# Optimization experiments

Hardware: AMD Instinct MI355X
Metric: run time of the kernel (lower is better)

## Reference

```python
import jax, jax.numpy as jnp
import numpy as np

E4M3_MAX = 448.0
CHUNKS = 4  # module init: chunks=4, seg_mode='weight', equal chunksizes of out//chunks


def fp8_quant(v):
    # Simulate real e4m3 quantization: saturate then round-to-nearest e4m3, back to f32.
    return jnp.clip(v, -E4M3_MAX, E4M3_MAX).astype(jnp.float8_e4m3fn).astype(jnp.float32)


def setup_inputs() -> dict:
    key = jax.random.key(0)
    k1, k2, k3 = jax.random.split(key, 3)
    B, S, IN, OUT = 4, 4096, 4096, 4096
    x = jax.random.normal(k1, (B, S, IN), jnp.float32)
    w = jax.random.normal(k2, (OUT, IN), jnp.float32) * 0.02
    bias = jax.random.normal(k3, (OUT,), jnp.float32) * 0.01
    # Max-calibrated per-tensor scales (quantizer.scale from calibration)
    in_scale = jnp.max(jnp.abs(x)) / E4M3_MAX          # scalar
    wc = w.reshape(CHUNKS, OUT // CHUNKS, IN)
    w_scales = jnp.max(jnp.abs(wc), axis=(1, 2)) / E4M3_MAX  # [CHUNKS]
    return {"x": x, "w": w, "bias": bias, "in_scale": in_scale, "w_scales": w_scales}


def reference(x, w, bias, in_scale, w_scales):
    # seg_mode='weight': split weight along out_features into CHUNKS equal chunks,
    # run scaled e4m3 GEMM per chunk, concat outputs along out dim, add bias.
    OUT, IN = w.shape
    wc = w.reshape(CHUNKS, OUT // CHUNKS, IN)                 # [c, oc, i]
    xq = fp8_quant(x / in_scale)                              # [b, s, i]
    wq = fp8_quant(wc / w_scales[:, None, None])              # [c, oc, i]
    # out_i = (xq @ wq_i^T) * in_scale * w_scale_i  (dequant fused into GEMM epilogue)
    out = jnp.einsum('bsi,coi->bsco', xq, wq)
    out = out * (in_scale * w_scales)[None, None, :, None]
    out = out.reshape(x.shape[0], x.shape[1], OUT)            # concat chunk outputs
    return out + bias
```

## Files before the change

kernel.cpp:

```cpp
#include <hip/hip_runtime.h>
#include <stdint.h>

#define E4M3_MAX 448.0f

typedef float f32x4 __attribute__((ext_vector_type(4)));
typedef int   i32x4 __attribute__((ext_vector_type(4)));
typedef int   i32x8 __attribute__((ext_vector_type(8)));

__device__ __forceinline__ void gload_lds16(const void* g, void* l) {
    __builtin_amdgcn_global_load_lds(
        (__attribute__((address_space(1))) void*)(void*)g,
        (__attribute__((address_space(3))) void*)l,
        16, 0, 0);
}

__device__ __forceinline__ uint32_t quant4(float a, float b, float c, float d) {
    a = fminf(fmaxf(a, -E4M3_MAX), E4M3_MAX);
    b = fminf(fmaxf(b, -E4M3_MAX), E4M3_MAX);
    c = fminf(fmaxf(c, -E4M3_MAX), E4M3_MAX);
    d = fminf(fmaxf(d, -E4M3_MAX), E4M3_MAX);
    int q = 0;
    q = __builtin_amdgcn_cvt_pk_fp8_f32(a, b, q, false);
    q = __builtin_amdgcn_cvt_pk_fp8_f32(c, d, q, true);
    return (uint32_t)q;
}

__global__ void quant_x_kernel(const float* __restrict__ x,
                               const float* __restrict__ scale_p,
                               uint4* __restrict__ xq, int n16) {
    const float inv = 1.0f / scale_p[0];
    const int stride = gridDim.x * blockDim.x;
    for (int i = blockIdx.x * blockDim.x + threadIdx.x; i < n16; i += stride) {
        const float4* p = (const float4*)x + (size_t)i * 4;
        float4 v0 = p[0], v1 = p[1], v2 = p[2], v3 = p[3];
        uint4 q;
        q.x = quant4(v0.x * inv, v0.y * inv, v0.z * inv, v0.w * inv);
        q.y = quant4(v1.x * inv, v1.y * inv, v1.z * inv, v1.w * inv);
        q.z = quant4(v2.x * inv, v2.y * inv, v2.z * inv, v2.w * inv);
        q.w = quant4(v3.x * inv, v3.y * inv, v3.z * inv, v3.w * inv);
        xq[i] = q;
    }
}

__global__ void quant_w_kernel(const float* __restrict__ w,
                               const float* __restrict__ wsc,
                               uint8_t* __restrict__ wq,
                               int Nrows, int K, int chunkRows) {
    const int nkt = K >> 7;
    const int n32 = Nrows * (K >> 5);
    const int stride = gridDim.x * blockDim.x;
    for (int i = blockIdx.x * blockDim.x + threadIdx.x; i < n32; i += stride) {
        const int n  = i % Nrows;
        const int k0 = (i / Nrows) << 5;
        const float inv = 1.0f / wsc[n / chunkRows];
        const float4* p = (const float4*)(w + (size_t)n * K + k0);
        uint4 qa, qb;
        {
            float4 v0 = p[0], v1 = p[1], v2 = p[2], v3 = p[3];
            qa.x = quant4(v0.x * inv, v0.y * inv, v0.z * inv, v0.w * inv);
            qa.y = quant4(v1.x * inv, v1.y * inv, v1.z * inv, v1.w * inv);
            qa.z = quant4(v2.x * inv, v2.y * inv, v2.z * inv, v2.w * inv);
            qa.w = quant4(v3.x * inv, v3.y * inv, v3.z * inv, v3.w * inv);
        }
        {
            float4 v0 = p[4], v1 = p[5], v2 = p[6], v3 = p[7];
            qb.x = quant4(v0.x * inv, v0.y * inv, v0.z * inv, v0.w * inv);
            qb.y = quant4(v1.x * inv, v1.y * inv, v1.z * inv, v1.w * inv);
            qb.z = quant4(v2.x * inv, v2.y * inv, v2.z * inv, v2.w * inv);
            qb.w = quant4(v3.x * inv, v3.y * inv, v3.z * inv, v3.w * inv);
        }
        const int kt = k0 >> 7, kg = (k0 >> 5) & 3, r = n & 15, nf = n >> 4;
        uint8_t* dst = wq + (((size_t)nf * nkt + kt) * 64 + kg * 16 + r) * 32;
        *(uint4*)dst = qa;
        *(uint4*)(dst + 16) = qb;
    }
}

__device__ __forceinline__ i32x8 read_frag(const uint8_t* base, int o0, int o1) {
    i32x4 lo = *(const i32x4*)(base + o0);
    i32x4 hi = *(const i32x4*)(base + o1);
    return __builtin_shufflevector(lo, hi, 0, 1, 2, 3, 4, 5, 6, 7);
}

#define MFMA_MX(a, b, c) \
    __builtin_amdgcn_mfma_scale_f32_16x16x128_f8f6f4( \
        (a), (b), (c), 0, 0, 0, 0x7F7F7F7F, 0, 0x7F7F7F7F)

#define WAIT_LGKM(n)                                            \
    do {                                                        \
        asm volatile("s_waitcnt lgkmcnt(" #n ")" ::: "memory"); \
        __builtin_amdgcn_sched_barrier(0);                      \
    } while (0)

#define BM 256
#define BN 256
#define BKB 128

__global__ __launch_bounds__(512, 2) void gemm_fp8_kernel(
    const uint8_t* __restrict__ Aq, const uint8_t* __restrict__ Bq,
    const float* __restrict__ bias, const float* __restrict__ isp,
    const float* __restrict__ wsc, float* __restrict__ out,
    int M, int N, int K, int ocPerChunk) {
    __shared__ __align__(16) uint8_t As[2][BM * BKB];

    const int tid  = threadIdx.x;
    const int lane = tid & 63;
    const int wid  = tid >> 6;
    const int wm   = wid >> 2;
    const int wn   = wid & 3;

    const int nbx   = N / BN;
    const int nby   = M / BM;
    const int chunk = nby >> 3;
    const int xcd   = blockIdx.x & 7;
    const int local = blockIdx.x >> 3;
    const int bx    = local / chunk;
    const int by    = xcd * chunk + (local % chunk);
    const int m0    = by * BM;
    const int n0    = bx * BN;

    const int lr   = lane & 15;
    const int sw   = (lr & 7) << 4;
    const int off0 = ((lane >> 4) * 32) ^ sw;
    const int off1 = off0 ^ 16;

    f32x4 acc[8][4] = {};

    const int nkt = K / BKB;

    const uint8_t* bbase =
        Bq + ((size_t)((n0 >> 4) + wn * 4) * nkt) * 2048 + lane * 32;

    auto stage = [&](int b, int kt) {
#pragma unroll
        for (int i = 0; i < 4; ++i) {
            const int idx = i * 512 + tid;
            const int row = idx >> 3;
            const int col = ((idx & 7) * 16) ^ ((row & 7) << 4);
            gload_lds16(Aq + (size_t)(m0 + row) * K + kt + col,
                        &As[b][0] + idx * 16);
        }
    };

    stage(0, 0);
    asm volatile("s_waitcnt vmcnt(0)" ::: "memory");
    __builtin_amdgcn_s_barrier();

    for (int t = 0; t < nkt; ++t) {
        const int cur = t & 1;
        const uint8_t* pa = &As[cur][0] + (wm * 128 + lr) * BKB;

        i32x8 bv[4];
#pragma unroll
        for (int ni = 0; ni < 4; ni++) {
            const uint8_t* p = bbase + ((size_t)ni * nkt + t) * 2048;
            i32x4 lo = *(const i32x4*)p;
            i32x4 hi = *(const i32x4*)(p + 16);
            bv[ni] = __builtin_shufflevector(lo, hi, 0, 1, 2, 3, 4, 5, 6, 7);
        }
        __builtin_amdgcn_sched_barrier(0);

        i32x8 a0 = read_frag(pa,            off0, off1);
        i32x8 a1 = read_frag(pa + 16 * BKB, off0, off1);
        i32x8 a2 = read_frag(pa + 32 * BKB, off0, off1);
        i32x8 a3 = read_frag(pa + 48 * BKB, off0, off1);
        __builtin_amdgcn_sched_barrier(0);
        const bool pre = (t + 1 < nkt);
        if (pre) stage(cur ^ 1, (t + 1) * BKB);
        __builtin_amdgcn_sched_barrier(0);

        if (pre) asm volatile("s_waitcnt vmcnt(4)" ::: "memory");
        else     asm volatile("s_waitcnt vmcnt(0)" ::: "memory");
        WAIT_LGKM(4);
        __builtin_amdgcn_s_setprio(1);
#pragma unroll
        for (int ni = 0; ni < 4; ni++) {
            acc[0][ni] = MFMA_MX(a0, bv[ni], acc[0][ni]);
            acc[1][ni] = MFMA_MX(a1, bv[ni], acc[1][ni]);
        }
        __builtin_amdgcn_s_setprio(0);

        i32x8 a4 = read_frag(pa + 64 * BKB, off0, off1);
        i32x8 a5 = read_frag(pa + 80 * BKB, off0, off1);
        WAIT_LGKM(4);
        __builtin_amdgcn_s_setprio(1);
#pragma unroll
        for (int ni = 0; ni < 4; ni++) {
            acc[2][ni] = MFMA_MX(a2, bv[ni], acc[2][ni]);
            acc[3][ni] = MFMA_MX(a3, bv[ni], acc[3][ni]);
        }
        __builtin_amdgcn_s_setprio(0);

        i32x8 a6 = read_frag(pa + 96 * BKB,  off0, off1);
        i32x8 a7 = read_frag(pa + 112 * BKB, off0, off1);
        WAIT_LGKM(4);
        __builtin_amdgcn_s_setprio(1);
#pragma unroll
        for (int ni = 0; ni < 4; ni++) {
            acc[4][ni] = MFMA_MX(a4, bv[ni], acc[4][ni]);
            acc[5][ni] = MFMA_MX(a5, bv[ni], acc[5][ni]);
        }
        __builtin_amdgcn_s_setprio(0);

        WAIT_LGKM(0);
        __builtin_amdgcn_s_setprio(1);
#pragma unroll
        for (int ni = 0; ni < 4; ni++) {
            acc[6][ni] = MFMA_MX(a6, bv[ni], acc[6][ni]);
            acc[7][ni] = MFMA_MX(a7, bv[ni], acc[7][ni]);
        }
        __builtin_amdgcn_s_setprio(0);

        asm volatile("s_waitcnt vmcnt(0)" ::: "memory");
        __builtin_amdgcn_sched_barrier(0);
        __builtin_amdgcn_s_barrier();
    }

    const float is = isp[0];
#pragma unroll
    for (int ni = 0; ni < 4; ni++) {
        const int cidx = n0 + wn * 64 + ni * 16 + lr;
        const float sc = is * wsc[cidx / ocPerChunk];
        const float bs = bias[cidx];
#pragma unroll
        for (int mi = 0; mi < 8; mi++) {
            const int rbase = m0 + wm * 128 + mi * 16 + (lane >> 4) * 4;
#pragma unroll
            for (int j = 0; j < 4; j++)
                out[(size_t)(rbase + j) * N + cidx] = acc[mi][ni][j] * sc + bs;
        }
    }
}

extern "C" void kernel_launch(void* const* d_in, const int* in_sizes, int n_in,
                              void* d_out, int out_size, void* d_ws, size_t ws_size,
                              hipStream_t stream) {
    const float* x        = (const float*)d_in[0];
    const float* w        = (const float*)d_in[1];
    const float* bias     = (const float*)d_in[2];
    const float* in_scale = (const float*)d_in[3];
    const float* w_scales = (const float*)d_in[4];
    float* out = (float*)d_out;

    const int N = in_sizes[2];
    const int K = in_sizes[1] / N;
    const int M = in_sizes[0] / K;
    const int CHUNKS = in_sizes[4];
    const int ocPerChunk = N / CHUNKS;

    uint8_t* xq = (uint8_t*)d_ws;
    uint8_t* wq = xq + (size_t)M * K;

    const int xn16 = (int)(((size_t)M * K) / 16);

    quant_x_kernel<<<2048, 256, 0, stream>>>(x, in_scale, (uint4*)xq, xn16);
    quant_w_kernel<<<2048, 256, 0, stream>>>(w, w_scales, wq, N, K, ocPerChunk);

    const int nblk = (M / BM) * (N / BN);
    gemm_fp8_kernel<<<dim3(nblk), 512, 0, stream>>>(xq, wq, bias, in_scale,
                                                    w_scales, out, M, N, K,
                                                    ocPerChunk);
}
```

Before: 422.2 us.

## Prefetch B fragments one K-tile ahead into double-buffered registers

B-operand fragments are now loaded from global memory one K-tile ahead, into a second set of registers, alongside the A-tile LDS stage. The loop is unrolled by two so the current and next register sets swap roles each half. The vmcnt waits are retuned so MFMAs no longer wait on the current tile's B loads, which hides global latency that used to be exposed every iteration. The cost is 32 more live VGPRs per lane under a launch bound of 2 blocks of 512 threads, which risks spills or lower occupancy. The loop also now assumes the number of K tiles is even.

```diff
diff --git a/kernel.cpp b/kernel.cpp
--- a/kernel.cpp
+++ b/kernel.cpp
@@ -82,6 +82,12 @@
     return __builtin_shufflevector(lo, hi, 0, 1, 2, 3, 4, 5, 6, 7);
 }
 
+__device__ __forceinline__ i32x8 load_bfrag(const uint8_t* p) {
+    i32x4 lo = *(const i32x4*)p;
+    i32x4 hi = *(const i32x4*)(p + 16);
+    return __builtin_shufflevector(lo, hi, 0, 1, 2, 3, 4, 5, 6, 7);
+}
+
 #define MFMA_MX(a, b, c) \
     __builtin_amdgcn_mfma_scale_f32_16x16x128_f8f6f4( \
         (a), (b), (c), 0, 0, 0, 0x7F7F7F7F, 0, 0x7F7F7F7F)
@@ -92,9 +98,88 @@
         __builtin_amdgcn_sched_barrier(0);                      \
     } while (0)
 
+#define WAIT_VM(n)                                              \
+    do {                                                        \
+        asm volatile("s_waitcnt vmcnt(" #n ")" ::: "memory");   \
+        __builtin_amdgcn_sched_barrier(0);                      \
+    } while (0)
+
 #define BM 256
 #define BN 256
 #define BKB 128
+
+#define TILE_ITER(T, BC0, BC1, BC2, BC3, BN0, BN1, BN2, BN3)                   \
+    do {                                                                       \
+        const int  cur = (T) & 1;                                              \
+        const bool pre = ((T) + 1 < nkt);                                      \
+        const uint8_t* pa = &As[cur][0] + (wm * 128 + lr) * BKB;               \
+        if (pre) {                                                             \
+            stage(cur ^ 1, ((T) + 1) * BKB);                                   \
+            __builtin_amdgcn_sched_barrier(0);                                 \
+            const uint8_t* bb = bbase + (size_t)((T) + 1) * 2048;              \
+            BN0 = load_bfrag(bb);                                              \
+            BN1 = load_bfrag(bb + (size_t)nkt * 2048);                         \
+            BN2 = load_bfrag(bb + (size_t)nkt * 4096);                         \
+            BN3 = load_bfrag(bb + (size_t)nkt * 6144);                         \
+            __builtin_amdgcn_sched_barrier(0);                                 \
+        }                                                                      \
+                            \
+        i32x8 a0 = read_frag(pa,            off0, off1);                       \
+        i32x8 a1 = read_frag(pa + 16 * BKB, off0, off1);                       \
+        i32x8 a2 = read_frag(pa + 32 * BKB, off0, off1);                       \
+        i32x8 a3 = read_frag(pa + 48 * BKB, off0, off1);                       \
+        if (pre) { WAIT_VM(12); } else { WAIT_VM(0); }                         \
+        WAIT_LGKM(4);                        \
+        __builtin_amdgcn_s_setprio(1);                                         \
+        acc[0][0] = MFMA_MX(a0, BC0, acc[0][0]);                               \
+        acc[0][1] = MFMA_MX(a0, BC1, acc[0][1]);                               \
+        acc[0][2] = MFMA_MX(a0, BC2, acc[0][2]);                               \
+        acc[0][3] = MFMA_MX(a0, BC3, acc[0][3]);                               \
+        acc[1][0] = MFMA_MX(a1, BC0, acc[1][0]);                               \
+        acc[1][1] = MFMA_MX(a1, BC1, acc[1][1]);                               \
+        acc[1][2] = MFMA_MX(a1, BC2, acc[1][2]);                               \
+        acc[1][3] = MFMA_MX(a1, BC3, acc[1][3]);                               \
+        __builtin_amdgcn_s_setprio(0);                                         \
+        i32x8 a4 = read_frag(pa + 64 * BKB, off0, off1);                       \
+        i32x8 a5 = read_frag(pa + 80 * BKB, off0, off1);                       \
+        WAIT_LGKM(4);                        \
+        __builtin_amdgcn_s_setprio(1);                                         \
+        acc[2][0] = MFMA_MX(a2, BC0, acc[2][0]);                               \
+        acc[2][1] = MFMA_MX(a2, BC1, acc[2][1]);                               \
+        acc[2][2] = MFMA_MX(a2, BC2, acc[2][2]);                               \
+        acc[2][3] = MFMA_MX(a2, BC3, acc[2][3]);                               \
+        acc[3][0] = MFMA_MX(a3, BC0, acc[3][0]);                               \
+        acc[3][1] = MFMA_MX(a3, BC1, acc[3][1]);                               \
+        acc[3][2] = MFMA_MX(a3, BC2, acc[3][2]);                               \
+        acc[3][3] = MFMA_MX(a3, BC3, acc[3][3]);                               \
+        __builtin_amdgcn_s_setprio(0);                                         \
+        i32x8 a6 = read_frag(pa + 96 * BKB,  off0, off1);                      \
+        i32x8 a7 = read_frag(pa + 112 * BKB, off0, off1);                      \
+        WAIT_LGKM(4);                        \
+        __builtin_amdgcn_s_setprio(1);                                         \
+        acc[4][0] = MFMA_MX(a4, BC0, acc[4][0]);                               \
+        acc[4][1] = MFMA_MX(a4, BC1, acc[4][1]);                               \
+        acc[4][2] = MFMA_MX(a4, BC2, acc[4][2]);                               \
+        acc[4][3] = MFMA_MX(a4, BC3, acc[4][3]);                               \
+        acc[5][0] = MFMA_MX(a5, BC0, acc[5][0]);                               \
+        acc[5][1] = MFMA_MX(a5, BC1, acc[5][1]);                               \
+        acc[5][2] = MFMA_MX(a5, BC2, acc[5][2]);                               \
+        acc[5][3] = MFMA_MX(a5, BC3, acc[5][3]);                               \
+        __builtin_amdgcn_s_setprio(0);                                         \
+        WAIT_LGKM(0);                                         \
+        __builtin_amdgcn_s_setprio(1);                                         \
+        acc[6][0] = MFMA_MX(a6, BC0, acc[6][0]);                               \
+        acc[6][1] = MFMA_MX(a6, BC1, acc[6][1]);                               \
+        acc[6][2] = MFMA_MX(a6, BC2, acc[6][2]);                               \
+        acc[6][3] = MFMA_MX(a6, BC3, acc[6][3]);                               \
+        acc[7][0] = MFMA_MX(a7, BC0, acc[7][0]);                               \
+        acc[7][1] = MFMA_MX(a7, BC1, acc[7][1]);                               \
+        acc[7][2] = MFMA_MX(a7, BC2, acc[7][2]);                               \
+        acc[7][3] = MFMA_MX(a7, BC3, acc[7][3]);                               \
+        __builtin_amdgcn_s_setprio(0);                                         \
+        if (pre) { WAIT_VM(8); } else { WAIT_VM(0); }                          \
+        __builtin_amdgcn_s_barrier();                                          \
+    } while (0)
 
 __global__ __launch_bounds__(512, 2) void gemm_fp8_kernel(
     const uint8_t* __restrict__ Aq, const uint8_t* __restrict__ Bq,
@@ -142,78 +227,19 @@
         }
     };
 
+    i32x8 bc0, bc1, bc2, bc3, bn0, bn1, bn2, bn3;
+
     stage(0, 0);
+    bc0 = load_bfrag(bbase);
+    bc1 = load_bfrag(bbase + (size_t)nkt * 2048);
+    bc2 = load_bfrag(bbase + (size_t)nkt * 4096);
+    bc3 = load_bfrag(bbase + (size_t)nkt * 6144);
     asm volatile("s_waitcnt vmcnt(0)" ::: "memory");
     __builtin_amdgcn_s_barrier();
 
-    for (int t = 0; t < nkt; ++t) {
-        const int cur = t & 1;
-        const uint8_t* pa = &As[cur][0] + (wm * 128 + lr) * BKB;
-
-        i32x8 bv[4];
-#pragma unroll
-        for (int ni = 0; ni < 4; ni++) {
-            const uint8_t* p = bbase + ((size_t)ni * nkt + t) * 2048;
-            i32x4 lo = *(const i32x4*)p;
-            i32x4 hi = *(const i32x4*)(p + 16);
-            bv[ni] = __builtin_shufflevector(lo, hi, 0, 1, 2, 3, 4, 5, 6, 7);
-        }
-        __builtin_amdgcn_sched_barrier(0);
-
-        i32x8 a0 = read_frag(pa,            off0, off1);
-        i32x8 a1 = read_frag(pa + 16 * BKB, off0, off1);
-        i32x8 a2 = read_frag(pa + 32 * BKB, off0, off1);
-        i32x8 a3 = read_frag(pa + 48 * BKB, off0, off1);
-        __builtin_amdgcn_sched_barrier(0);
-        const bool pre = (t + 1 < nkt);
-        if (pre) stage(cur ^ 1, (t + 1) * BKB);
-        __builtin_amdgcn_sched_barrier(0);
-
-        if (pre) asm volatile("s_waitcnt vmcnt(4)" ::: "memory");
-        else     asm volatile("s_waitcnt vmcnt(0)" ::: "memory");
-        WAIT_LGKM(4);
-        __builtin_amdgcn_s_setprio(1);
-#pragma unroll
-        for (int ni = 0; ni < 4; ni++) {
-            acc[0][ni] = MFMA_MX(a0, bv[ni], acc[0][ni]);
-            acc[1][ni] = MFMA_MX(a1, bv[ni], acc[1][ni]);
-        }
-        __builtin_amdgcn_s_setprio(0);
-
-        i32x8 a4 = read_frag(pa + 64 * BKB, off0, off1);
-        i32x8 a5 = read_frag(pa + 80 * BKB, off0, off1);
-        WAIT_LGKM(4);
-        __builtin_amdgcn_s_setprio(1);
-#pragma unroll
-        for (int ni = 0; ni < 4; ni++) {
-            acc[2][ni] = MFMA_MX(a2, bv[ni], acc[2][ni]);
-            acc[3][ni] = MFMA_MX(a3, bv[ni], acc[3][ni]);
-        }
-        __builtin_amdgcn_s_setprio(0);
-
-        i32x8 a6 = read_frag(pa + 96 * BKB,  off0, off1);
-        i32x8 a7 = read_frag(pa + 112 * BKB, off0, off1);
-        WAIT_LGKM(4);
-        __builtin_amdgcn_s_setprio(1);
-#pragma unroll
-        for (int ni = 0; ni < 4; ni++) {
-            acc[4][ni] = MFMA_MX(a4, bv[ni], acc[4][ni]);
-            acc[5][ni] = MFMA_MX(a5, bv[ni], acc[5][ni]);
-        }
-        __builtin_amdgcn_s_setprio(0);
-
-        WAIT_LGKM(0);
-        __builtin_amdgcn_s_setprio(1);
-#pragma unroll
-        for (int ni = 0; ni < 4; ni++) {
-            acc[6][ni] = MFMA_MX(a6, bv[ni], acc[6][ni]);
-            acc[7][ni] = MFMA_MX(a7, bv[ni], acc[7][ni]);
-        }
-        __builtin_amdgcn_s_setprio(0);
-
-        asm volatile("s_waitcnt vmcnt(0)" ::: "memory");
-        __builtin_amdgcn_sched_barrier(0);
-        __builtin_amdgcn_s_barrier();
+    for (int t = 0; t < nkt; t += 2) {
+        TILE_ITER(t,     bc0, bc1, bc2, bc3, bn0, bn1, bn2, bn3);
+        TILE_ITER(t + 1, bn0, bn1, bn2, bn3, bc0, bc1, bc2, bc3);
     }
 
     const float is = isp[0];
```

Result: slower. 1.664 ms (+294.2%).
